# Optimization experiments

Hardware: AMD Instinct MI355X
Metric: run time of the kernel (lower is better)

The kernel has to match this reference:

```python
import jax, jax.numpy as jnp
import numpy as np

# physical constants (init_kwargs)
M1 = 1.0; M2 = 1.0; M3 = 1.0
L1 = 1.0; L2 = 1.0; L3 = 1.0
G = 9.81


def _kin(td):
    # td: [6] = (theta1, theta2, theta3, dth1, dth2, dth3)
    th, dth = td[:3], td[3:]
    dx1 = dth[0] * L1 * jnp.cos(th[0])
    dy1 = dth[0] * L1 * jnp.sin(th[0])
    dx2 = dx1 + dth[1] * L2 * jnp.cos(th[1])
    dy2 = dy1 + dth[1] * L2 * jnp.sin(th[1])
    dx3 = dx2 + dth[2] * L3 * jnp.cos(th[2])
    dy3 = dy2 + dth[2] * L3 * jnp.sin(th[2])
    vs1 = dx1 * dx1 + dy1 * dy1
    vs2 = dx2 * dx2 + dy2 * dy2
    vs3 = dx3 * dx3 + dy3 * dy3
    return 0.5 * (M1 * vs1 + M2 * vs2 + M3 * vs3)


def _pot(td):
    th = td[:3]
    y1 = -L1 * jnp.cos(th[0])
    y2 = y1 - L2 * jnp.cos(th[1])
    y3 = y2 - L3 * jnp.cos(th[2])
    return (M1 * G * (y1 + L1)
            + M2 * G * (y2 + L1 + L2)
            + M3 * G * (y3 + L1 + L2 + L3))


def _hamiltonian(y):
    # y: [6] = (theta, p_theta). Mass matrix = Hessian of kin w.r.t. velocity slots.
    Mmat = jax.hessian(_kin)(y)[3:6, 3:6]          # 3x3 mass matrix M(theta)
    p = y[3:6]
    dth = p @ jnp.linalg.inv(Mmat)                 # p_theta -> d_theta (M symmetric)
    K = _kin(jnp.concatenate([y[:3], dth]))
    return K + _pot(y)


def _dyn(y):
    g = jax.grad(_hamiltonian)(y)                  # dH/d(theta,p)
    return jnp.concatenate([g[3:6], -g[:3]])       # (dq, dp)


def setup_inputs() -> dict:
    key = jax.random.key(0)
    y = jax.random.normal(key, (2097152, 6), dtype=jnp.float32)
    t = jnp.zeros((1,), dtype=jnp.float32)
    return {"t": t, "y": y}


def reference(t, y):
    # t is unused by the dynamics (autonomous system), kept for API fidelity.
    return jax.vmap(_dyn)(y)
```

## Files before the change

### kernel.cpp

```cpp
#include <hip/hip_runtime.h>


#define GACC 9.81f

__device__ __forceinline__ void dyn6(float th1, float th2, float th3,
                                     float p1, float p2, float p3,
                                     float* __restrict__ o) {
    float s1, c1, s2, c2, s3, c3;
    __sincosf(th1, &s1, &c1);
    __sincosf(th2, &s2, &c2);
    __sincosf(th3, &s3, &c3);
    float c12 = c1 * c2 + s1 * s2, s12 = s1 * c2 - c1 * s2;
    float c13 = c1 * c3 + s1 * s3, s13 = s1 * c3 - c1 * s3;
    float c23 = c2 * c3 + s2 * s3, s23 = s2 * c3 - c2 * s3;
    float A11 = 2.0f - c23 * c23;
    float A12 = c23 * c13 - 2.0f * c12;
    float A13 = 2.0f * (c12 * c23 - c13);
    float A22 = 3.0f - c13 * c13;
    float A23 = 2.0f * c12 * c13 - 3.0f * c23;
    float A33 = 6.0f - 4.0f * c12 * c12;
    float det = 3.0f * A11 + 2.0f * c12 * A12 + c13 * A13;
    float inv = 1.0f / det;
    float dth1 = (A11 * p1 + A12 * p2 + A13 * p3) * inv;
    float dth2 = (A12 * p1 + A22 * p2 + A23 * p3) * inv;
    float dth3 = (A13 * p1 + A23 * p2 + A33 * p3) * inv;
    o[0] = dth1;
    o[1] = dth2;
    o[2] = dth3;
    float t12 = dth1 * dth2 * s12;
    float t13 = dth1 * dth3 * s13;
    float t23 = dth2 * dth3 * s23;
    o[3] = -2.0f * t12 - t13 - 3.0f * GACC * s1;
    o[4] =  2.0f * t12 - t23 - 2.0f * GACC * s2;
    o[5] =  t13 + t23 - GACC * s3;
}

__device__ __forceinline__ int swz(int j) { return j ^ ((j >> 3) & 3); }

__global__ __launch_bounds__(256) void pend3_kernel(const float4* __restrict__ y4,
                                                    float4* __restrict__ out4) {
    __shared__ float4 sIn[768];
    __shared__ float4 sOut[768];
    const int tid = threadIdx.x;
    const size_t base = (size_t)blockIdx.x * 768;

#pragma unroll
    for (int k = 0; k < 3; ++k) {
        int j = tid + k * 256;
        sIn[swz(j)] = y4[base + j];
    }
    __syncthreads();

    const int j0 = 3 * tid;
    float4 a = sIn[swz(j0)];
    float4 b = sIn[swz(j0 + 1)];
    float4 c = sIn[swz(j0 + 2)];

    float o0[6], o1[6];
    dyn6(a.x, a.y, a.z, a.w, b.x, b.y, o0);
    dyn6(b.z, b.w, c.x, c.y, c.z, c.w, o1);

    sOut[swz(j0)]     = make_float4(o0[0], o0[1], o0[2], o0[3]);
    sOut[swz(j0 + 1)] = make_float4(o0[4], o0[5], o1[0], o1[1]);
    sOut[swz(j0 + 2)] = make_float4(o1[2], o1[3], o1[4], o1[5]);
    __syncthreads();

#pragma unroll
    for (int k = 0; k < 3; ++k) {
        int j = tid + k * 256;
        out4[base + j] = sOut[swz(j)];
    }
}

extern "C" void kernel_launch(void* const* d_in, const int* in_sizes, int n_in,
                              void* d_out, int out_size, void* d_ws, size_t ws_size,
                              hipStream_t stream) {
    const float4* y4 = (const float4*)d_in[1];
    float4* out4 = (float4*)d_out;
    int nQuads = in_sizes[1] / 4;
    int grid = nQuads / 768;
    pend3_kernel<<<grid, 256, 0, stream>>>(y4, out4);
}
```

Measured before the change: 20.86 us.

## Use per-wave LDS staging, persistent grid-stride tiles, and nontemporal stores

Each wavefront now stages its own 192-quad slice in LDS and orders the accesses with wavefront fences instead of block-wide barriers. One shared buffer replaces the separate input and output buffers, and the XOR swizzle is removed. The grid is capped at 2048 blocks that loop over tiles, and output goes through nontemporal stores. This is meant to cut barrier stalls, LDS footprint and launch overhead, but it risks LDS bank conflicts on the stride-3 accesses now that the swizzle is gone, and fewer blocks may hide memory latency less well.

```diff
diff --git a/kernel.cpp b/kernel.cpp
--- a/kernel.cpp
+++ b/kernel.cpp
@@ -2,6 +2,8 @@
 
 
 #define GACC 9.81f
+
+typedef float f32x4 __attribute__((ext_vector_type(4)));
 
 __device__ __forceinline__ void dyn6(float th1, float th2, float th3,
                                      float p1, float p2, float p3,
@@ -35,49 +37,57 @@
     o[5] =  t13 + t23 - GACC * s3;
 }
 
-__device__ __forceinline__ int swz(int j) { return j ^ ((j >> 3) & 3); }
+#define WFENCE() __builtin_amdgcn_fence(__ATOMIC_SEQ_CST, "wavefront")
 
-__global__ __launch_bounds__(256) void pend3_kernel(const float4* __restrict__ y4,
-                                                    float4* __restrict__ out4) {
-    __shared__ float4 sIn[768];
-    __shared__ float4 sOut[768];
-    const int tid = threadIdx.x;
-    const size_t base = (size_t)blockIdx.x * 768;
+__global__ __launch_bounds__(256, 6) void pend3_kernel(const f32x4* __restrict__ y4,
+                                                       f32x4* __restrict__ out4,
+                                                       int nTiles) {
+    __shared__ f32x4 s[768];
+    const int wave = threadIdx.x >> 6;
+    const int lane = threadIdx.x & 63;
+    f32x4* sw = s + wave * 192;
+
+    for (int tile = blockIdx.x; tile < nTiles; tile += gridDim.x) {
+        const size_t gbase = (size_t)tile * 768 + wave * 192;
 
 #pragma unroll
-    for (int k = 0; k < 3; ++k) {
-        int j = tid + k * 256;
-        sIn[swz(j)] = y4[base + j];
-    }
-    __syncthreads();
+        for (int k = 0; k < 3; ++k)
+            sw[lane + 64 * k] = y4[gbase + lane + 64 * k];
+        WFENCE();
 
-    const int j0 = 3 * tid;
-    float4 a = sIn[swz(j0)];
-    float4 b = sIn[swz(j0 + 1)];
-    float4 c = sIn[swz(j0 + 2)];
+        const int j0 = 3 * lane;
+        f32x4 a = sw[j0];
+        f32x4 b = sw[j0 + 1];
+        f32x4 c = sw[j0 + 2];
 
-    float o0[6], o1[6];
-    dyn6(a.x, a.y, a.z, a.w, b.x, b.y, o0);
-    dyn6(b.z, b.w, c.x, c.y, c.z, c.w, o1);
+        float o0[6], o1[6];
+        dyn6(a.x, a.y, a.z, a.w, b.x, b.y, o0);
+        dyn6(b.z, b.w, c.x, c.y, c.z, c.w, o1);
 
-    sOut[swz(j0)]     = make_float4(o0[0], o0[1], o0[2], o0[3]);
-    sOut[swz(j0 + 1)] = make_float4(o0[4], o0[5], o1[0], o1[1]);
-    sOut[swz(j0 + 2)] = make_float4(o1[2], o1[3], o1[4], o1[5]);
-    __syncthreads();
+        f32x4 r0 = {o0[0], o0[1], o0[2], o0[3]};
+        f32x4 r1 = {o0[4], o0[5], o1[0], o1[1]};
+        f32x4 r2 = {o1[2], o1[3], o1[4], o1[5]};
+        sw[j0]     = r0;
+        sw[j0 + 1] = r1;
+        sw[j0 + 2] = r2;
+        WFENCE();
 
 #pragma unroll
-    for (int k = 0; k < 3; ++k) {
-        int j = tid + k * 256;
-        out4[base + j] = sOut[swz(j)];
+        for (int k = 0; k < 3; ++k) {
+            f32x4 v = sw[lane + 64 * k];
+            __builtin_nontemporal_store(v, &out4[gbase + lane + 64 * k]);
+        }
+        WFENCE();
     }
 }
 
 extern "C" void kernel_launch(void* const* d_in, const int* in_sizes, int n_in,
                               void* d_out, int out_size, void* d_ws, size_t ws_size,
                               hipStream_t stream) {
-    const float4* y4 = (const float4*)d_in[1];
-    float4* out4 = (float4*)d_out;
+    const f32x4* y4 = (const f32x4*)d_in[1];
+    f32x4* out4 = (f32x4*)d_out;
     int nQuads = in_sizes[1] / 4;
-    int grid = nQuads / 768;
-    pend3_kernel<<<grid, 256, 0, stream>>>(y4, out4);
+    int nTiles = nQuads / 768;
+    int grid = nTiles < 2048 ? nTiles : 2048;
+    pend3_kernel<<<grid, 256, 0, stream>>>(y4, out4, nTiles);
 }
```

New measurement: 20.82 us. Within noise of the previous version (-0.2%).
